# Kernel tuning notes

Hardware: AMD Instinct MI355X
Metric: run time of the kernel (lower is better)

Reference implementation:

```python
import jax, jax.numpy as jnp
import numpy as np

N = 10000      # miRNA_numbers (nodes)
E = 320000     # similarity-graph edges (avg degree 32)
M = 4          # modalities / channel_num (doc, role, tpcp, ernie)
D = 256        # per-modality feature dim (doc_dim=role_dim=tpcp_dim=ernie_dim)
P = 256        # pro_dim
NEG_SLOPE = 0.2  # PyG GATConv default negative_slope


def setup_inputs() -> dict:
    key = jax.random.key(0)
    ks = jax.random.split(key, 10)
    s = 1.0 / np.sqrt(D).astype(np.float32)
    return {
        "x_feats": jax.random.normal(ks[0], (M, N, D), jnp.float32),
        "edge_index": jax.random.randint(ks[1], (2, E), 0, N, dtype=jnp.int32),
        "Wg": jax.random.normal(ks[2], (M, D, D), jnp.float32) * s,      # GAT lin weights
        "a_src": jax.random.normal(ks[3], (M, D), jnp.float32) * s,      # GAT att_src
        "a_dst": jax.random.normal(ks[4], (M, D), jnp.float32) * s,      # GAT att_dst
        "bg": jnp.zeros((M, D), jnp.float32),                            # GAT bias
        "Wp": jax.random.normal(ks[5], (M, D, P), jnp.float32) * s,      # per-modality Linear(d, pro_dim)
        "bp": jnp.zeros((M, P), jnp.float32),
        "conv_w": jax.random.normal(ks[6], (M,), jnp.float32) * 0.5,     # 1x1 Conv2d channel mixer
        "conv_b": jnp.zeros((), jnp.float32),
    }


def reference(x_feats, edge_index, Wg, a_src, a_dst, bg, Wp, bp, conv_w, conv_b):
    n = x_feats.shape[1]
    loop = jnp.arange(n, dtype=edge_index.dtype)
    # PyG GATConv adds self-loops by default
    src = jnp.concatenate([edge_index[0], loop])  # [E+N]
    dst = jnp.concatenate([edge_index[1], loop])  # [E+N]

    def gat(x, W, asrc, adst, b):
        h = x @ W                                            # [N, D]
        alpha = (h * asrc).sum(-1)[src] + (h * adst).sum(-1)[dst]
        alpha = jax.nn.leaky_relu(alpha, NEG_SLOPE)          # [E+N]
        mx = jax.ops.segment_max(alpha, dst, num_segments=n)
        e = jnp.exp(alpha - mx[dst])
        denom = jax.ops.segment_sum(e, dst, num_segments=n) + 1e-16
        coef = e / denom[dst]                                # edge softmax per destination
        out = jax.ops.segment_sum(h[src] * coef[:, None], dst, num_segments=n)
        return out + b

    # 4 modality GATs over the same graph (eval mode: dropout = identity)
    h = jax.nn.relu(jax.vmap(gat)(x_feats, Wg, a_src, a_dst, bg))      # [M, N, D]
    xp = jnp.einsum('mnd,mdp->mnp', h, Wp) + bp[:, None, :]            # per-modality projection
    # 1x1 conv channel fusion across the M modality channels
    fused = jnp.einsum('m,mnp->np', conv_w, xp) + conv_b               # [N, P]
    return fused
```

## Files before the change

### kernel.cpp

```cpp
#include <hip/hip_runtime.h>
#include <hip/hip_bf16.h>
#include <hip/hip_fp16.h>
#include <cstdint>
#include <cstddef>

constexpr int kN = 10000;
constexpr int kE = 320000;
constexpr int kM = 4;
constexpr int kD = 256;
constexpr int kP = 256;
constexpr float kSlope = 0.2f;
constexpr int kCap = 96;

typedef __attribute__((ext_vector_type(8))) short bf16x8;
typedef __attribute__((ext_vector_type(4))) float f32x4;
typedef __attribute__((ext_vector_type(2))) float f32x2;

__device__ __forceinline__ unsigned short f2bf(float f) {
  union { float ff; unsigned int i; } v; v.ff = f;
  unsigned int x = v.i;
  unsigned int r = x + 0x7fffu + ((x >> 16) & 1u);
  return (unsigned short)(r >> 16);
}
__device__ __forceinline__ uint4 pack8(float4 a, float4 b) {
  uint4 o;
  o.x = (unsigned)f2bf(a.x) | ((unsigned)f2bf(a.y) << 16);
  o.y = (unsigned)f2bf(a.z) | ((unsigned)f2bf(a.w) << 16);
  o.z = (unsigned)f2bf(b.x) | ((unsigned)f2bf(b.y) << 16);
  o.w = (unsigned)f2bf(b.z) | ((unsigned)f2bf(b.w) << 16);
  return o;
}
__device__ __forceinline__ void gload_lds16(const void* g, void* l) {
  __builtin_amdgcn_global_load_lds((const __attribute__((address_space(1))) unsigned int*)g,
                                   (__attribute__((address_space(3))) unsigned int*)l, 16, 0, 0);
}


__global__ __launch_bounds__(256) void weight_prep_kernel(
    const float* __restrict__ Wg, const float* __restrict__ bp,
    const float* __restrict__ cw, const float* __restrict__ cb,
    unsigned short* __restrict__ Wgt, float* __restrict__ biasp, int* __restrict__ cnt) {
  const int blk = blockIdx.x;
  if (blk >= 65) {
    int z = blk - 65;
    int t = threadIdx.x;
    if (t < 250) ((int4*)cnt)[z * 250 + t] = make_int4(0, 0, 0, 0);
    return;
  }
  if (blk == 64) {
    int p = threadIdx.x;
    float v = cb[0];
#pragma unroll
    for (int mm = 0; mm < kM; mm++) v += cw[mm] * bp[mm * kP + p];
    biasp[p] = v;
    return;
  }
  __shared__ float tile[64][65];
  const int m = blk >> 4;
  const int t2 = blk & 15;
  const int r0 = (t2 >> 2) * 64;
  const int c0 = (t2 & 3) * 64;
  const float* in = Wg + ((size_t)m << 16);
#pragma unroll
  for (int l = 0; l < 16; l++) {
    int idx = l * 256 + threadIdx.x;
    int rr = idx >> 6, cc = idx & 63;
    tile[rr][cc] = in[(size_t)(c0 + rr) * 256 + r0 + cc];
  }
  __syncthreads();
#pragma unroll
  for (int l = 0; l < 16; l++) {
    int idx = l * 256 + threadIdx.x;
    int rr = idx >> 6, cc = idx & 63;
    Wgt[((size_t)m << 16) + (size_t)(r0 + rr) * 256 + c0 + cc] = f2bf(tile[cc][rr]);
  }
}


constexpr int ASTR = 64 * 8 + 8;
constexpr int BSTR = 256 * 8 + 8;
constexpr int kAsBytes = 2 * 4 * ASTR * 2;
constexpr int kBsBytes = 2 * 4 * BSTR * 2;

__global__ __launch_bounds__(256) void gemm_h_csr_mfma(
    const float* __restrict__ x, const unsigned short* __restrict__ Wgt,
    const float* __restrict__ asrc, const float* __restrict__ adst,
    const int* __restrict__ ei, int* __restrict__ cnt, int* __restrict__ csr_src,
    const float* __restrict__ Wp, const float* __restrict__ cw,
    unsigned short* __restrict__ Wqt,
    unsigned short* __restrict__ hb, float* __restrict__ sv, float* __restrict__ tv) {
  const int blk = blockIdx.x;
  const int tid = threadIdx.x;

  __shared__ __align__(16) char smem[kAsBytes + kBsBytes];
  __shared__ float sred[256], tred[256];
  auto As = (unsigned short(*)[4 * ASTR])smem;
  auto Bs = (unsigned short(*)[4 * BSTR])(smem + kAsBytes);

  if (blk >= 945) {
    auto tile = (float(*)[65])smem;
    const int b = blk - 945;
    const int m = b >> 4;
    const int t2 = b & 15;
    const int r0 = (t2 >> 2) * 64;
    const int c0 = (t2 & 3) * 64;
    const float* in = Wp + ((size_t)m << 16);
    const float scale = cw[m];
#pragma unroll
    for (int l = 0; l < 16; l++) {
      int idx = l * 256 + tid;
      int rr = idx >> 6, cc = idx & 63;
      tile[rr][cc] = in[(size_t)(c0 + rr) * 256 + r0 + cc] * scale;
    }
    __syncthreads();
#pragma unroll
    for (int l = 0; l < 16; l++) {
      int idx = l * 256 + tid;
      int rr = idx >> 6, cc = idx & 63;
      Wqt[(size_t)(r0 + rr) * 1024 + (m << 8) + c0 + cc] = f2bf(tile[cc][rr]);
    }
    return;
  }

  if (blk >= 632) {
    int t = (blk - 632) * 256 + tid;
    int e4 = t * 4;
    if (e4 >= kE) return;
    int4 s4 = *(const int4*)&ei[e4];
    int4 d4 = *(const int4*)&ei[kE + e4];
    int sl;
    sl = atomicAdd(&cnt[d4.x], 1); csr_src[d4.x * kCap + sl] = s4.x;
    sl = atomicAdd(&cnt[d4.y], 1); csr_src[d4.y * kCap + sl] = s4.y;
    sl = atomicAdd(&cnt[d4.z], 1); csr_src[d4.z * kCap + sl] = s4.z;
    sl = atomicAdd(&cnt[d4.w], 1); csr_src[d4.w * kCap + sl] = s4.w;
    return;
  }

  const int m = (blk & 7) >> 1;
  const int i = (blk >> 3) * 2 + (blk & 1);
  if (i >= 157) return;
  const int row0 = i * 64;

  const int wave = tid >> 6, lane = tid & 63;
  const int lidx = lane & 15, lslot = lane >> 4;
  const int wcol0 = wave * 64;

  const int arow_s = tid & 63, aslot_s = tid >> 6;
  const int agr = min(row0 + arow_s, kN - 1);
  const float* Abase = x + ((size_t)m * kN + agr) * kD + aslot_s * 8;
  const unsigned short* Bbase = Wgt + (size_t)m * kD * kD;

  f32x4 acc[4][4] = {};

  {
    float4 f0 = *(const float4*)(Abase);
    float4 f1 = *(const float4*)(Abase + 4);
    *(uint4*)&As[0][aslot_s * ASTR + arow_s * 8] = pack8(f0, f1);
#pragma unroll
    for (int l = 0; l < 4; l++) {
      int c = tid + l * 256;
      int col = c & 255, slot = c >> 8;
      gload_lds16(Bbase + (size_t)col * kD + slot * 8, &Bs[0][slot * BSTR + col * 8]);
    }
  }
  __syncthreads();

  int buf = 0;
  for (int t = 0; t < 8; t++) {
    float4 f0, f1;
    const bool pf = (t < 7);
    if (pf) {
      const int k1 = (t + 1) * 32;
      f0 = *(const float4*)(Abase + k1);
      f1 = *(const float4*)(Abase + k1 + 4);
#pragma unroll
      for (int l = 0; l < 4; l++) {
        int c = tid + l * 256;
        int col = c & 255, slot = c >> 8;
        gload_lds16(Bbase + (size_t)col * kD + k1 + slot * 8,
                    &Bs[buf ^ 1][slot * BSTR + col * 8]);
      }
    }
    bf16x8 a[4], bfr[4];
#pragma unroll
    for (int i2 = 0; i2 < 4; i2++)
      a[i2] = *(const bf16x8*)&As[buf][lslot * ASTR + (i2 * 16 + lidx) * 8];
#pragma unroll
    for (int j = 0; j < 4; j++)
      bfr[j] = *(const bf16x8*)&Bs[buf][lslot * BSTR + (wcol0 + j * 16 + lidx) * 8];
#pragma unroll
    for (int i2 = 0; i2 < 4; i2++)
#pragma unroll
      for (int j = 0; j < 4; j++)
        acc[i2][j] = __builtin_amdgcn_mfma_f32_16x16x32_bf16(a[i2], bfr[j], acc[i2][j], 0, 0, 0);
    if (pf) {
      *(uint4*)&As[buf ^ 1][aslot_s * ASTR + arow_s * 8] = pack8(f0, f1);
    }
    __syncthreads();
    buf ^= 1;
  }

  const int slot4 = lane >> 4;
  float av[4], dv[4];
#pragma unroll
  for (int j = 0; j < 4; j++) {
    av[j] = asrc[m * kD + wcol0 + j * 16 + lidx];
    dv[j] = adst[m * kD + wcol0 + j * 16 + lidx];
  }
#pragma unroll
  for (int i2 = 0; i2 < 4; i2++) {
#pragma unroll
    for (int reg = 0; reg < 4; reg++) {
      int grow = row0 + i2 * 16 + slot4 * 4 + reg;
      float sp = 0.f, tp = 0.f;
#pragma unroll
      for (int j = 0; j < 4; j++) {
        float hv = acc[i2][j][reg];
        sp += hv * av[j];
        tp += hv * dv[j];
        if (grow < kN)
          hb[((size_t)m * kN + grow) * kD + wcol0 + j * 16 + lidx] =
              __half_as_ushort(__float2half(hv));
      }
#pragma unroll
      for (int o = 1; o < 16; o <<= 1) {
        sp += __shfl_xor(sp, o);
        tp += __shfl_xor(tp, o);
      }
      if (lidx == 0) {
        sred[wave * 64 + i2 * 16 + slot4 * 4 + reg] = sp;
        tred[wave * 64 + i2 * 16 + slot4 * 4 + reg] = tp;
      }
    }
  }
  __syncthreads();
  if (tid < 64) {
    int grow = row0 + tid;
    if (grow < kN) {
      float s = sred[tid] + sred[64 + tid] + sred[128 + tid] + sred[192 + tid];
      float t = tred[tid] + tred[64 + tid] + tred[128 + tid] + tred[192 + tid];
      sv[m * kN + grow] = s;
      tv[m * kN + grow] = t;
    }
  }
}


__global__ __launch_bounds__(256) void gat_aggregate_kernel(
    const unsigned short* __restrict__ hb, const float* __restrict__ sv,
    const float* __restrict__ tv, const float* __restrict__ bg,
    const int* __restrict__ cnt, const int* __restrict__ csr_src,
    unsigned short* __restrict__ hrelb) {
  const int l = blockIdx.x;
  const int xcd = l & 7;
  const int m = xcd >> 1;
  const int ngroup = (l >> 3) * 2 + (xcd & 1);
  const int wv = threadIdx.x >> 6;
  const int n = ngroup * 4 + wv;
  const int lane = threadIdx.x & 63;
  const int half = lane >> 5;
  const int lf = lane & 31;
  const int fb = lf * 8;
  const unsigned fbyte = (unsigned)lf * 16u;

  __shared__ uint2 ebuf[4][64];

  const float tt = tv[m * kN + n];
  const int b = n * kCap;
  const int deg = cnt[n];

  float a_self = sv[m * kN + n] + tt;
  a_self = fmaxf(a_self, kSlope * a_self);
  const float e_self = __expf(a_self);

  const char* hmB = (const char*)(hb + ((size_t)m * kN << 8));

  __half2 cacc[4];
  cacc[0] = cacc[1] = cacc[2] = cacc[3] = __float2half2_rn(0.f);
  {
    const __half2 es2 = __float2half2_rn(half ? 0.f : e_self);
    uint4 hx = *(const uint4*)(hmB + (((unsigned)n << 9) + fbyte));
#pragma unroll
    for (int q = 0; q < 4; q++) {
      unsigned w = ((const unsigned*)&hx)[q];
      __half2 hv2 = *reinterpret_cast<const __half2*>(&w);
      cacc[q] = __hfma2(hv2, es2, cacc[q]);
    }
  }
  float denom = (lane == 0) ? e_self : 0.f;

  for (int c0 = 0; c0 < deg; c0 += 64) {
    int j = c0 + lane;
    float ee = 0.f;
    unsigned soff = 0;
    if (j < deg) {
      int src = csr_src[b + j];
      float a = sv[m * kN + src] + tt;
      a = fmaxf(a, kSlope * a);
      ee = __expf(a);
      soff = (unsigned)src << 9;
    }
    denom += ee;
    union { __half2 h2; unsigned u; } ec;
    ec.h2 = __float2half2_rn(ee);
    ebuf[wv][lane] = make_uint2(ec.u, soff);
    const int cl = min(64, deg - c0);
    const uint2* ebase = &ebuf[wv][half];
    for (int j2 = 0; j2 < cl; j2 += 8) {
#pragma unroll
      for (int p = 0; p < 4; p++) {
        uint2 es_ = ebase[j2 + 2 * p];
        __half2 ep2 = *reinterpret_cast<const __half2*>(&es_.x);
        uint4 hx = *(const uint4*)(hmB + (es_.y + fbyte));
#pragma unroll
        for (int q = 0; q < 4; q++) {
          unsigned w = ((const unsigned*)&hx)[q];
          __half2 hv2 = *reinterpret_cast<const __half2*>(&w);
          cacc[q] = __hfma2(hv2, ep2, cacc[q]);
        }
      }
    }
  }
#pragma unroll
  for (int o = 32; o > 0; o >>= 1) denom += __shfl_xor(denom, o);
  const float inv = 1.f / (denom + 1e-16f);

  f32x2 acc2[4];
#pragma unroll
  for (int q = 0; q < 4; q++) {
    float2 f = __half22float2(cacc[q]);
    acc2[q].x = f.x + __shfl_xor(f.x, 32);
    acc2[q].y = f.y + __shfl_xor(f.y, 32);
  }

  if (half == 0) {
    const float* bgp = bg + m * kD + fb;
    float4 b0 = *(const float4*)bgp;
    float4 b1 = *(const float4*)(bgp + 4);
    float4 o0, o1;
    o0.x = fmaxf(acc2[0].x * inv + b0.x, 0.f);
    o0.y = fmaxf(acc2[0].y * inv + b0.y, 0.f);
    o0.z = fmaxf(acc2[1].x * inv + b0.z, 0.f);
    o0.w = fmaxf(acc2[1].y * inv + b0.w, 0.f);
    o1.x = fmaxf(acc2[2].x * inv + b1.x, 0.f);
    o1.y = fmaxf(acc2[2].y * inv + b1.y, 0.f);
    o1.z = fmaxf(acc2[3].x * inv + b1.z, 0.f);
    o1.w = fmaxf(acc2[3].y * inv + b1.w, 0.f);
    *(uint4*)(hrelb + (((size_t)m * kN + n) << 8) + fb) = pack8(o0, o1);
  }
}


constexpr int FSTR = 64 * 8 + 8;

__global__ __launch_bounds__(256) void gemm_fused_mfma(const unsigned short* __restrict__ hrelb,
                                                       const unsigned short* __restrict__ Wqt,
                                                       const float* __restrict__ biasp,
                                                       float* __restrict__ out) {
  const int l = blockIdx.x;
  const int xcd = l & 7;
  const int t0 = l >> 3;
  const int c = t0 & 3;
  const int r = (t0 >> 2) * 8 + xcd;
  if (r >= 157) return;
  const int row0 = r * 64;
  const int col0 = c * 64;

  const int tid = threadIdx.x;
  const int wave = tid >> 6, lane = tid & 63;
  const int lidx = lane & 15, lslot = lane >> 4;
  const int wr = wave >> 1, wc = wave & 1;

  __shared__ __align__(16) unsigned short As[2][8 * FSTR];
  __shared__ __align__(16) unsigned short Bs[2][8 * FSTR];

  f32x4 acc[2][2] = {};

  const int arow = min(row0 + (tid & 63), kN - 1);
  const int bcol = col0 + (tid & 63);

#pragma unroll
  for (int ll = 0; ll < 2; ll++) {
    int slot = (tid >> 6) + ll * 4;
    gload_lds16(hrelb + ((size_t)arow << 8) + slot * 8,
                &As[0][slot * FSTR + (tid & 63) * 8]);
    gload_lds16(Wqt + (size_t)bcol * 1024 + slot * 8,
                &Bs[0][slot * FSTR + (tid & 63) * 8]);
  }
  __syncthreads();

  int buf = 0;
  for (int t = 0; t < 16; t++) {
    if (t < 15) {
      const int k1 = (t + 1) * 64;
      const int mm = k1 >> 8;
      const int d1 = k1 & 255;
#pragma unroll
      for (int ll = 0; ll < 2; ll++) {
        int slot = (tid >> 6) + ll * 4;
        gload_lds16(hrelb + (((size_t)mm * kN + arow) << 8) + d1 + slot * 8,
                    &As[buf ^ 1][slot * FSTR + (tid & 63) * 8]);
        gload_lds16(Wqt + (size_t)bcol * 1024 + k1 + slot * 8,
                    &Bs[buf ^ 1][slot * FSTR + (tid & 63) * 8]);
      }
    }
#pragma unroll
    for (int s = 0; s < 2; s++) {
      const int ks = s * 4 + lslot;
      bf16x8 a[2], bfr[2];
#pragma unroll
      for (int i = 0; i < 2; i++)
        a[i] = *(const bf16x8*)&As[buf][ks * FSTR + (wr * 32 + i * 16 + lidx) * 8];
#pragma unroll
      for (int j = 0; j < 2; j++)
        bfr[j] = *(const bf16x8*)&Bs[buf][ks * FSTR + (wc * 32 + j * 16 + lidx) * 8];
#pragma unroll
      for (int i = 0; i < 2; i++)
#pragma unroll
        for (int j = 0; j < 2; j++)
          acc[i][j] = __builtin_amdgcn_mfma_f32_16x16x32_bf16(a[i], bfr[j], acc[i][j], 0, 0, 0);
    }
    __syncthreads();
    buf ^= 1;
  }

  const int slot4 = lane >> 4;
#pragma unroll
  for (int i = 0; i < 2; i++) {
#pragma unroll
    for (int reg = 0; reg < 4; reg++) {
      int grow = row0 + wr * 32 + i * 16 + slot4 * 4 + reg;
      if (grow < kN) {
#pragma unroll
        for (int j = 0; j < 2; j++) {
          int gcol = col0 + wc * 32 + j * 16 + lidx;
          out[(size_t)grow * kP + gcol] = acc[i][j][reg] + biasp[gcol];
        }
      }
    }
  }
}


extern "C" void kernel_launch(void* const* d_in, const int* in_sizes, int n_in,
                              void* d_out, int out_size, void* d_ws, size_t ws_size,
                              hipStream_t stream) {
  const float* x = (const float*)d_in[0];
  const int* ei = (const int*)d_in[1];
  const float* Wg = (const float*)d_in[2];
  const float* asrc = (const float*)d_in[3];
  const float* adst = (const float*)d_in[4];
  const float* bg = (const float*)d_in[5];
  const float* Wp = (const float*)d_in[6];
  const float* bp = (const float*)d_in[7];
  const float* cw = (const float*)d_in[8];
  const float* cb = (const float*)d_in[9];
  float* out = (float*)d_out;

  char* ws = (char*)d_ws;
  size_t off = 0;
  auto alloc = [&](size_t bytes) -> void* {
    void* p = ws + off;
    off = (off + bytes + 255) & ~(size_t)255;
    return p;
  };
  unsigned short* hb = (unsigned short*)alloc((size_t)kM * kN * kD * 2);
  unsigned short* hrelb = (unsigned short*)alloc((size_t)kM * kN * kD * 2);
  unsigned short* Wgt = (unsigned short*)alloc((size_t)kM * kD * kD * 2);
  unsigned short* Wqt = (unsigned short*)alloc((size_t)kP * kM * kD * 2);
  float* sv = (float*)alloc((size_t)kM * kN * sizeof(float));
  float* tv = (float*)alloc((size_t)kM * kN * sizeof(float));
  float* biasp = (float*)alloc(kP * sizeof(float));
  int* cnt = (int*)alloc(kN * sizeof(int));
  int* csr_src = (int*)alloc((size_t)kN * kCap * sizeof(int));

  weight_prep_kernel<<<75, 256, 0, stream>>>(Wg, bp, cw, cb, Wgt, biasp, cnt);

  gemm_h_csr_mfma<<<1009, 256, 0, stream>>>(x, Wgt, asrc, adst, ei, cnt, csr_src,
                                            Wp, cw, Wqt, hb, sv, tv);

  gat_aggregate_kernel<<<kN, 256, 0, stream>>>(hb, sv, tv, bg, cnt, csr_src, hrelb);

  gemm_fused_mfma<<<640, 256, 0, stream>>>(hrelb, Wqt, biasp, out);
}
```

Measured before the change: 114.0 us.

## Store weights and hidden features in k-blocked layout for coalesced LDS loads

The transposed bf16 weights (Wgt, Wqt) and the relu'd GAT output (hrelb) are now stored as [k/8][row][8] blocks instead of row-major. The direct-to-LDS loads in both GEMMs then read contiguous 16-byte chunks across threads, where before each thread read a strided column. The A-tile thread mapping in the first GEMM is also changed so consecutive threads read adjacent k-slots of the same row. This touches the producer and consumer kernels together, so an index mismatch would silently corrupt results.

```diff
diff --git a/kernel.cpp b/kernel.cpp
--- a/kernel.cpp
+++ b/kernel.cpp
@@ -11,6 +11,7 @@
 constexpr int kP = 256;
 constexpr float kSlope = 0.2f;
 constexpr int kCap = 96;
+
 
 typedef __attribute__((ext_vector_type(8))) short bf16x8;
 typedef __attribute__((ext_vector_type(4))) float f32x4;
@@ -72,7 +73,8 @@
   for (int l = 0; l < 16; l++) {
     int idx = l * 256 + threadIdx.x;
     int rr = idx >> 6, cc = idx & 63;
-    Wgt[((size_t)m << 16) + (size_t)(r0 + rr) * 256 + c0 + cc] = f2bf(tile[cc][rr]);
+    int j = r0 + rr, k = c0 + cc;
+    Wgt[((size_t)m << 16) + ((k >> 3) << 11) + j * 8 + (k & 7)] = f2bf(tile[cc][rr]);
   }
 }
 
@@ -117,7 +119,9 @@
     for (int l = 0; l < 16; l++) {
       int idx = l * 256 + tid;
       int rr = idx >> 6, cc = idx & 63;
-      Wqt[(size_t)(r0 + rr) * 1024 + (m << 8) + c0 + cc] = f2bf(tile[cc][rr]);
+      int p = r0 + rr;
+      int q = (m << 8) + c0 + cc;
+      Wqt[((q >> 3) << 11) + p * 8 + (q & 7)] = f2bf(tile[cc][rr]);
     }
     return;
   }
@@ -145,10 +149,10 @@
   const int lidx = lane & 15, lslot = lane >> 4;
   const int wcol0 = wave * 64;
 
-  const int arow_s = tid & 63, aslot_s = tid >> 6;
+  const int arow_s = tid >> 2, aslot_s = tid & 3;
   const int agr = min(row0 + arow_s, kN - 1);
   const float* Abase = x + ((size_t)m * kN + agr) * kD + aslot_s * 8;
-  const unsigned short* Bbase = Wgt + (size_t)m * kD * kD;
+  const unsigned short* Bbase = Wgt + ((size_t)m << 16);
 
   f32x4 acc[4][4] = {};
 
@@ -158,9 +162,7 @@
     *(uint4*)&As[0][aslot_s * ASTR + arow_s * 8] = pack8(f0, f1);
 #pragma unroll
     for (int l = 0; l < 4; l++) {
-      int c = tid + l * 256;
-      int col = c & 255, slot = c >> 8;
-      gload_lds16(Bbase + (size_t)col * kD + slot * 8, &Bs[0][slot * BSTR + col * 8]);
+      gload_lds16(Bbase + ((size_t)l << 11) + tid * 8, &Bs[0][l * BSTR + tid * 8]);
     }
   }
   __syncthreads();
@@ -173,12 +175,11 @@
       const int k1 = (t + 1) * 32;
       f0 = *(const float4*)(Abase + k1);
       f1 = *(const float4*)(Abase + k1 + 4);
+      const int kb1 = (t + 1) * 4;
 #pragma unroll
       for (int l = 0; l < 4; l++) {
-        int c = tid + l * 256;
-        int col = c & 255, slot = c >> 8;
-        gload_lds16(Bbase + (size_t)col * kD + k1 + slot * 8,
-                    &Bs[buf ^ 1][slot * BSTR + col * 8]);
+        gload_lds16(Bbase + ((size_t)(kb1 + l) << 11) + tid * 8,
+                    &Bs[buf ^ 1][l * BSTR + tid * 8]);
       }
     }
     bf16x8 a[4], bfr[4];
@@ -346,7 +347,7 @@
     o1.y = fmaxf(acc2[2].y * inv + b1.y, 0.f);
     o1.z = fmaxf(acc2[3].x * inv + b1.z, 0.f);
     o1.w = fmaxf(acc2[3].y * inv + b1.w, 0.f);
-    *(uint4*)(hrelb + (((size_t)m * kN + n) << 8) + fb) = pack8(o0, o1);
+    *(uint4*)(hrelb + (((size_t)(m * 32 + lf)) * kN + n) * 8) = pack8(o0, o1);
   }
 }
 
@@ -382,9 +383,9 @@
 #pragma unroll
   for (int ll = 0; ll < 2; ll++) {
     int slot = (tid >> 6) + ll * 4;
-    gload_lds16(hrelb + ((size_t)arow << 8) + slot * 8,
+    gload_lds16(hrelb + ((size_t)slot * kN + arow) * 8,
                 &As[0][slot * FSTR + (tid & 63) * 8]);
-    gload_lds16(Wqt + (size_t)bcol * 1024 + slot * 8,
+    gload_lds16(Wqt + ((size_t)slot << 11) + bcol * 8,
                 &Bs[0][slot * FSTR + (tid & 63) * 8]);
   }
   __syncthreads();
@@ -392,15 +393,13 @@
   int buf = 0;
   for (int t = 0; t < 16; t++) {
     if (t < 15) {
-      const int k1 = (t + 1) * 64;
-      const int mm = k1 >> 8;
-      const int d1 = k1 & 255;
+      const int kb1 = (t + 1) * 8;
 #pragma unroll
       for (int ll = 0; ll < 2; ll++) {
         int slot = (tid >> 6) + ll * 4;
-        gload_lds16(hrelb + (((size_t)mm * kN + arow) << 8) + d1 + slot * 8,
+        gload_lds16(hrelb + ((size_t)(kb1 + slot) * kN + arow) * 8,
                     &As[buf ^ 1][slot * FSTR + (tid & 63) * 8]);
-        gload_lds16(Wqt + (size_t)bcol * 1024 + k1 + slot * 8,
+        gload_lds16(Wqt + ((size_t)(kb1 + slot) << 11) + bcol * 8,
                     &Bs[buf ^ 1][slot * FSTR + (tid & 63) * 8]);
       }
     }
```

Measured after the change: 102.2 us. -10.4%, faster.
